# Kernel tuning notes

Hardware: AMD Instinct MI355X
Metric: run time of the kernel (lower is better)

## Reference

```python
import jax, jax.numpy as jnp
import numpy as np

NUM_EMB = 81920
EMB_DIM = 64


def setup_inputs() -> dict:
    key = jax.random.key(0)
    k1, k2 = jax.random.split(key)
    z = jax.random.normal(k1, (4, 8, 8, 8, EMB_DIM), dtype=jnp.float32)
    # faithful to nn.Embedding init: uniform(-1/K, 1/K)
    emb = jax.random.uniform(k2, (NUM_EMB, EMB_DIM), dtype=jnp.float32,
                             minval=-1.0 / NUM_EMB, maxval=1.0 / NUM_EMB)
    return {"z": z, "emb": emb}


def reference(z, emb):
    bs, h, w, d, c = z.shape
    zf = z.reshape(-1, c)  # [N, C]
    # squared euclidean distances; argmin identical to cdist argmin
    # [N, K] = ||z||^2 - 2 z.E^T + ||E||^2
    d2 = (jnp.sum(zf * zf, axis=-1, keepdims=True)
          - 2.0 * jnp.einsum('nc,kc->nk', zf, emb)
          + jnp.sum(emb * emb, axis=-1))
    idx = jnp.argmin(d2, axis=1)  # [N]
    quantized = emb[idx].reshape(bs, h, w, d, c)
    commitment_loss = jnp.mean((z - jax.lax.stop_gradient(quantized)) ** 2)
    vq_loss = jnp.mean((quantized - jax.lax.stop_gradient(z)) ** 2)
    quantized_st = z + jax.lax.stop_gradient(quantized - z)
    return quantized_st, vq_loss, commitment_loss, idx.reshape(bs, h, w, d)
```

## Files before the change

### kernel.cpp

```cpp
#include <hip/hip_runtime.h>
#include <stdint.h>

#define NQ 2048
#define KK 81920
#define CD 64
#define CAP 64
#define DMARG 1.6e-5f
#define QPB 128
#define NSLICE 160
#define SPX 20
#define SPB 5
#define NQBLK 16

#define OUT_VQ 131072
#define OUT_CM 131073
#define OUT_IDX 131074

#define WS_QMAX 0
#define WS_CNT  8192
#define WS_KEYS 16384
#define WS_LOSS 32768
#define WS_CAND 33024
#define WS_ZBF  589824
#define WS_EBF  851968
#define WS_BMAX 11337728

typedef short v8s __attribute__((ext_vector_type(8)));
typedef float v4f __attribute__((ext_vector_type(4)));

__device__ __forceinline__ unsigned int f2o(float f) {
  unsigned int u = __float_as_uint(f);
  return (u & 0x80000000u) ? ~u : (u | 0x80000000u);
}
__device__ __forceinline__ float o2f(unsigned int u) {
  unsigned int v = (u & 0x80000000u) ? (u & 0x7FFFFFFFu) : ~u;
  return __uint_as_float(v);
}
__device__ __forceinline__ unsigned int bf16rne(float f) {
  unsigned int u = __float_as_uint(f);
  u = u + 0x7FFFu + ((u >> 16) & 1u);
  return u >> 16;
}

#define NZ4 32768
#define NTOT4 1343488
__global__ __launch_bounds__(256) void convert_kernel(
    const float* __restrict__ z, const float* __restrict__ emb,
    unsigned int* __restrict__ zbf, unsigned int* __restrict__ ebf,
    int* __restrict__ cnt, float* __restrict__ loss) {
  const int gid = blockIdx.x * 256 + threadIdx.x;
  if (gid < NQ) cnt[gid] = 0;
  if (gid == NQ) *loss = 0.0f;
  const int stride = gridDim.x * 256;
#pragma unroll 1
  for (int i = gid; i < NTOT4; i += stride) {
    const bool isz = (i < NZ4);
    const float4 v = isz ? ((const float4*)z)[i] : ((const float4*)emb)[i - NZ4];
    uint2 o;
    o.x = bf16rne(v.x) | (bf16rne(v.y) << 16);
    o.y = bf16rne(v.z) | (bf16rne(v.w) << 16);
    if (isz) ((uint2*)zbf)[i] = o;
    else     ((uint2*)ebf)[i - NZ4] = o;
  }
}

struct BlkMap { int q0, slice0, xcd, sgrp; };
__device__ __forceinline__ BlkMap decode_block(int bid) {
  BlkMap m;
  m.xcd = bid & 7;
  const int i = bid >> 3;
  const int qblk = i & 15;
  m.sgrp = i >> 4;
  m.q0 = qblk * QPB;
  m.slice0 = m.xcd * SPX + m.sgrp * SPB;
  return m;
}

__device__ __forceinline__ void load_B(v8s (&Bb)[8][2],
                                       const unsigned short* __restrict__ ebf,
                                       int code0, int lrow, int quad) {
#pragma unroll
  for (int cg = 0; cg < 8; ++cg) {
    const unsigned short* er = ebf + (size_t)(code0 + cg * 16 + lrow) * CD + quad * 8;
    Bb[cg][0] = *(const v8s*)er;
    Bb[cg][1] = *(const v8s*)(er + 32);
  }
}

__global__ __launch_bounds__(256, 2) void pass1_kernel(
    const unsigned short* __restrict__ zbf, const unsigned short* __restrict__ ebf,
    unsigned int* __restrict__ bmax) {
  const int tid = threadIdx.x;
  const int wave = tid >> 6, lane = tid & 63;
  const int quad = lane >> 4, lrow = lane & 15;
  const BlkMap bm = decode_block(blockIdx.x);

  v8s A0[8], A1[8];
#pragma unroll
  for (int qg = 0; qg < 8; ++qg) {
    const unsigned short* zr = zbf + (size_t)(bm.q0 + qg * 16 + lrow) * CD + quad * 8;
    A0[qg] = *(const v8s*)zr;
    A1[qg] = *(const v8s*)(zr + 32);
  }

  float pmax[8][4];
#pragma unroll
  for (int qg = 0; qg < 8; ++qg)
#pragma unroll
    for (int r = 0; r < 4; ++r) pmax[qg][r] = -1e30f;

#pragma unroll 1
  for (int s = 0; s < SPB; ++s) {
    v8s B[8][2];
    load_B(B, ebf, (bm.slice0 + s) * 512 + wave * 128, lrow, quad);
#pragma unroll
    for (int qg = 0; qg < 8; ++qg) {
#pragma unroll
      for (int cg = 0; cg < 8; ++cg) {
        v4f acc = {0.f, 0.f, 0.f, 0.f};
        acc = __builtin_amdgcn_mfma_f32_16x16x32_bf16(A0[qg], B[cg][0], acc, 0, 0, 0);
        acc = __builtin_amdgcn_mfma_f32_16x16x32_bf16(A1[qg], B[cg][1], acc, 0, 0, 0);
#pragma unroll
        for (int r = 0; r < 4; ++r) pmax[qg][r] = fmaxf(pmax[qg][r], acc[r]);
      }
    }
  }

#pragma unroll
  for (int m = 1; m <= 8; m <<= 1)
#pragma unroll
    for (int qg = 0; qg < 8; ++qg)
#pragma unroll
      for (int r = 0; r < 4; ++r)
        pmax[qg][r] = fmaxf(pmax[qg][r], __shfl_xor(pmax[qg][r], m, 64));

  __shared__ unsigned int smax[4][QPB];
  if (lrow == 0) {
#pragma unroll
    for (int qg = 0; qg < 8; ++qg) {
      uint4 v;
      v.x = f2o(pmax[qg][0]); v.y = f2o(pmax[qg][1]);
      v.z = f2o(pmax[qg][2]); v.w = f2o(pmax[qg][3]);
      *(uint4*)&smax[wave][qg * 16 + quad * 4] = v;
    }
  }
  __syncthreads();
  if (tid < QPB) {
    unsigned int m0 = smax[0][tid], m1 = smax[1][tid];
    unsigned int m2 = smax[2][tid], m3 = smax[3][tid];
    unsigned int m01 = m0 > m1 ? m0 : m1;
    unsigned int m23 = m2 > m3 ? m2 : m3;
    bmax[(size_t)(bm.q0 + tid) * 32 + bm.xcd * 4 + bm.sgrp] = m01 > m23 ? m01 : m23;
  }
}

__global__ __launch_bounds__(256) void reduce_qmax_kernel(
    const unsigned int* __restrict__ bmax, unsigned int* __restrict__ qmax) {
  const int t = threadIdx.x;
  const int q = blockIdx.x * 8 + (t >> 5);
  const int j = t & 31;
  unsigned int m = bmax[(size_t)q * 32 + j];
#pragma unroll
  for (int s = 16; s; s >>= 1) {
    unsigned int o = (unsigned int)__shfl_xor((int)m, s, 64);
    m = m > o ? m : o;
  }
  if (j == 0) qmax[q] = m;
}

__global__ __launch_bounds__(256, 2) void collect_kernel(
    const unsigned short* __restrict__ zbf, const unsigned short* __restrict__ ebf,
    const unsigned int* __restrict__ qmax, int* __restrict__ cnt,
    int* __restrict__ cand) {
  const int tid = threadIdx.x;
  const int wave = tid >> 6, lane = tid & 63;
  const int quad = lane >> 4, lrow = lane & 15;
  const BlkMap bm = decode_block(blockIdx.x);

  v8s A0[8], A1[8];
#pragma unroll
  for (int qg = 0; qg < 8; ++qg) {
    const unsigned short* zr = zbf + (size_t)(bm.q0 + qg * 16 + lrow) * CD + quad * 8;
    A0[qg] = *(const v8s*)zr;
    A1[qg] = *(const v8s*)(zr + 32);
  }
  float thr[8][4];
#pragma unroll
  for (int qg = 0; qg < 8; ++qg) {
    const uint4 tv = *(const uint4*)(qmax + bm.q0 + qg * 16 + quad * 4);
    thr[qg][0] = o2f(tv.x) - DMARG; thr[qg][1] = o2f(tv.y) - DMARG;
    thr[qg][2] = o2f(tv.z) - DMARG; thr[qg][3] = o2f(tv.w) - DMARG;
  }

#pragma unroll 1
  for (int s = 0; s < SPB; ++s) {
    v8s B[8][2];
    const int scode0 = (bm.slice0 + s) * 512 + wave * 128;
    load_B(B, ebf, scode0, lrow, quad);
#pragma unroll
    for (int qg = 0; qg < 8; ++qg) {
#pragma unroll
      for (int cg = 0; cg < 8; ++cg) {
        v4f acc = {0.f, 0.f, 0.f, 0.f};
        acc = __builtin_amdgcn_mfma_f32_16x16x32_bf16(A0[qg], B[cg][0], acc, 0, 0, 0);
        acc = __builtin_amdgcn_mfma_f32_16x16x32_bf16(A1[qg], B[cg][1], acc, 0, 0, 0);
        const float m01 = fmaxf(acc[0] - thr[qg][0], acc[1] - thr[qg][1]);
        const float m23 = fmaxf(acc[2] - thr[qg][2], acc[3] - thr[qg][3]);
        if (fmaxf(m01, m23) >= 0.0f) {
          const int code = scode0 + cg * 16 + lrow;
#pragma unroll
          for (int r = 0; r < 4; ++r) {
            if (acc[r] >= thr[qg][r]) {
              const int q = bm.q0 + qg * 16 + quad * 4 + r;
              const int pos = atomicAdd(&cnt[q], 1);
              if (pos < CAP) cand[q * CAP + pos] = code;
            }
          }
        }
      }
    }
  }
}

__device__ __forceinline__ unsigned long long exact_key(
    const float* __restrict__ emb, const float zr[CD], float zn2, int k) {
#pragma clang fp contract(off)
  float er[CD];
  const float4* ep = (const float4*)(emb + (size_t)k * CD);
#pragma unroll
  for (int j = 0; j < 16; ++j) {
    float4 v = ep[j];
    er[4 * j] = v.x; er[4 * j + 1] = v.y; er[4 * j + 2] = v.z; er[4 * j + 3] = v.w;
  }
  float acc[16];
#pragma unroll
  for (int j = 0; j < 16; ++j) acc[j] = 0.0f;
#pragma unroll
  for (int q4 = 0; q4 < 16; ++q4) {
    const int jb = 4 * (q4 & 3), cb = 4 * q4;
    acc[jb + 0] = __builtin_fmaf(er[cb + 0], zr[cb + 0], acc[jb + 0]);
    acc[jb + 1] = __builtin_fmaf(er[cb + 1], zr[cb + 1], acc[jb + 1]);
    acc[jb + 2] = __builtin_fmaf(er[cb + 2], zr[cb + 2], acc[jb + 2]);
    acc[jb + 3] = __builtin_fmaf(er[cb + 3], zr[cb + 3], acc[jb + 3]);
  }
  float b8[8], b4[4];
#pragma unroll
  for (int j = 0; j < 8; ++j) b8[j] = acc[j] + acc[j + 8];
#pragma unroll
  for (int j = 0; j < 4; ++j) b4[j] = b8[j] + b8[j + 4];
  const float dot = (b4[0] + b4[2]) + (b4[1] + b4[3]);
  const float t = zn2 - 2.0f * dot;
  return ((unsigned long long)f2o(t) << 32) | (unsigned int)k;
}

__global__ __launch_bounds__(256) void rescore_finalize_kernel(
    const float* __restrict__ z, const float* __restrict__ emb,
    const int* __restrict__ cnt, const int* __restrict__ cand,
    unsigned long long* __restrict__ keys, float* __restrict__ out,
    float* __restrict__ loss) {
#pragma clang fp contract(off)
  const int t = threadIdx.x;
  const int wv = t >> 6, lane = t & 63;
  const int n = blockIdx.x * 4 + wv;

  float zr[CD];
  {
    const float4* zp = (const float4*)(z + (size_t)n * CD);
#pragma unroll
    for (int i = 0; i < 16; ++i) {
      float4 v = zp[i];
      zr[4 * i] = v.x; zr[4 * i + 1] = v.y; zr[4 * i + 2] = v.z; zr[4 * i + 3] = v.w;
    }
  }
  float zn2;
  {
    float r[8];
#pragma unroll
    for (int j = 0; j < 8; ++j) r[j] = zr[j] * zr[j];
#pragma unroll
    for (int i = 8; i < CD; i += 8)
#pragma unroll
      for (int j = 0; j < 8; ++j) r[j] += zr[i + j] * zr[i + j];
    zn2 = ((r[0] + r[1]) + (r[2] + r[3])) + ((r[4] + r[5]) + (r[6] + r[7]));
  }

  const int c = cnt[n];
  unsigned long long best = ~0ull;
  if (c <= CAP) {
    if (lane < c) best = exact_key(emb, zr, zn2, cand[n * CAP + lane]);
  } else {
#pragma unroll 1
    for (int k = lane; k < KK; k += 64) {
      unsigned long long key = exact_key(emb, zr, zn2, k);
      best = (key < best) ? key : best;
    }
  }
#pragma unroll
  for (int m = 32; m; m >>= 1) {
    unsigned long long o = __shfl_xor(best, m, 64);
    best = (o < best) ? o : best;
  }
  const int idx = (int)(best & 0xFFFFFFFFull);
  if (lane == 0) keys[n] = best;

  const float e = emb[(size_t)idx * CD + lane];
  const float zv = z[(size_t)n * CD + lane];
  const float dst = e - zv;
  out[(size_t)n * CD + lane] = zv + dst;
  if (lane == 0) out[OUT_IDX + n] = (float)idx;
  float d = zv - e;
  float sq = d * d;
#pragma unroll
  for (int off = 32; off > 0; off >>= 1) sq += __shfl_down(sq, off, 64);
  __shared__ float part[4];
  if (lane == 0) part[wv] = sq;
  __syncthreads();
  if (t == 0) atomicAdd(loss, part[0] + part[1] + part[2] + part[3]);
}

__global__ void write_losses(const float* __restrict__ loss, float* __restrict__ out) {
  float m = *loss / (float)(NQ * CD);
  out[OUT_VQ] = m;
  out[OUT_CM] = m;
}

extern "C" void kernel_launch(void* const* d_in, const int* in_sizes, int n_in,
                              void* d_out, int out_size, void* d_ws, size_t ws_size,
                              hipStream_t stream) {
  const float* z = (const float*)d_in[0];
  const float* emb = (const float*)d_in[1];
  float* out = (float*)d_out;
  char* ws = (char*)d_ws;
  unsigned int* qmax = (unsigned int*)(ws + WS_QMAX);
  int* cnt = (int*)(ws + WS_CNT);
  unsigned long long* keys = (unsigned long long*)(ws + WS_KEYS);
  float* loss = (float*)(ws + WS_LOSS);
  int* cand = (int*)(ws + WS_CAND);
  unsigned int* zbf = (unsigned int*)(ws + WS_ZBF);
  unsigned int* ebf = (unsigned int*)(ws + WS_EBF);
  unsigned int* bmax = (unsigned int*)(ws + WS_BMAX);

  convert_kernel<<<1312, 256, 0, stream>>>(z, emb, zbf, ebf, cnt, loss);
  pass1_kernel<<<512, 256, 0, stream>>>(
      (const unsigned short*)zbf, (const unsigned short*)ebf, bmax);
  reduce_qmax_kernel<<<NQ / 8, 256, 0, stream>>>(bmax, qmax);
  collect_kernel<<<512, 256, 0, stream>>>(
      (const unsigned short*)zbf, (const unsigned short*)ebf, qmax, cnt, cand);
  rescore_finalize_kernel<<<NQ / 4, 256, 0, stream>>>(z, emb, cnt, cand, keys, out, loss);
  write_losses<<<1, 1, 0, stream>>>(loss, out);
}
```

Before: 152.1 us.

## Double-buffer codebook loads in pass1/collect and fold qmax reduction into collect

Splits each 128-code B tile into two halves and prefetches the next slice's half while MFMAs run on the other, so global loads overlap with compute in both pass1 and collect. It also removes the separate reduce_qmax kernel: each collect block now reduces its 128 queries' 32 partial maxima into shared memory itself. The unused keys write from rescore is dropped. The prefetch keeps two half-tiles live at once, which may raise register pressure under the 2-blocks-per-SM launch bound, and collect redundantly recomputes qmax in every block.

```diff
diff --git a/kernel.cpp b/kernel.cpp
--- a/kernel.cpp
+++ b/kernel.cpp
@@ -76,12 +76,12 @@
   return m;
 }
 
-__device__ __forceinline__ void load_B(v8s (&Bb)[8][2],
-                                       const unsigned short* __restrict__ ebf,
-                                       int code0, int lrow, int quad) {
-#pragma unroll
-  for (int cg = 0; cg < 8; ++cg) {
-    const unsigned short* er = ebf + (size_t)(code0 + cg * 16 + lrow) * CD + quad * 8;
+__device__ __forceinline__ void load_Bhalf(v8s (&Bb)[4][2],
+                                           const unsigned short* __restrict__ ebf,
+                                           int codeh0, int lrow, int quad) {
+#pragma unroll
+  for (int cg = 0; cg < 4; ++cg) {
+    const unsigned short* er = ebf + (size_t)(codeh0 + cg * 16 + lrow) * CD + quad * 8;
     Bb[cg][0] = *(const v8s*)er;
     Bb[cg][1] = *(const v8s*)(er + 32);
   }
@@ -109,21 +109,39 @@
 #pragma unroll
     for (int r = 0; r < 4; ++r) pmax[qg][r] = -1e30f;
 
+  v8s B0[4][2], B1[4][2];
+  {
+    const int c0 = bm.slice0 * 512 + wave * 128;
+    load_Bhalf(B0, ebf, c0, lrow, quad);
+    load_Bhalf(B1, ebf, c0 + 64, lrow, quad);
+  }
 #pragma unroll 1
   for (int s = 0; s < SPB; ++s) {
-    v8s B[8][2];
-    load_B(B, ebf, (bm.slice0 + s) * 512 + wave * 128, lrow, quad);
-#pragma unroll
-    for (int qg = 0; qg < 8; ++qg) {
-#pragma unroll
-      for (int cg = 0; cg < 8; ++cg) {
+    const int cnext = (bm.slice0 + s + 1) * 512 + wave * 128;
+#pragma unroll
+    for (int qg = 0; qg < 8; ++qg) {
+#pragma unroll
+      for (int cg = 0; cg < 4; ++cg) {
         v4f acc = {0.f, 0.f, 0.f, 0.f};
-        acc = __builtin_amdgcn_mfma_f32_16x16x32_bf16(A0[qg], B[cg][0], acc, 0, 0, 0);
-        acc = __builtin_amdgcn_mfma_f32_16x16x32_bf16(A1[qg], B[cg][1], acc, 0, 0, 0);
+        acc = __builtin_amdgcn_mfma_f32_16x16x32_bf16(A0[qg], B0[cg][0], acc, 0, 0, 0);
+        acc = __builtin_amdgcn_mfma_f32_16x16x32_bf16(A1[qg], B0[cg][1], acc, 0, 0, 0);
 #pragma unroll
         for (int r = 0; r < 4; ++r) pmax[qg][r] = fmaxf(pmax[qg][r], acc[r]);
       }
     }
+    if (s + 1 < SPB) load_Bhalf(B0, ebf, cnext, lrow, quad);
+#pragma unroll
+    for (int qg = 0; qg < 8; ++qg) {
+#pragma unroll
+      for (int cg = 0; cg < 4; ++cg) {
+        v4f acc = {0.f, 0.f, 0.f, 0.f};
+        acc = __builtin_amdgcn_mfma_f32_16x16x32_bf16(A0[qg], B1[cg][0], acc, 0, 0, 0);
+        acc = __builtin_amdgcn_mfma_f32_16x16x32_bf16(A1[qg], B1[cg][1], acc, 0, 0, 0);
+#pragma unroll
+        for (int r = 0; r < 4; ++r) pmax[qg][r] = fmaxf(pmax[qg][r], acc[r]);
+      }
+    }
+    if (s + 1 < SPB) load_Bhalf(B1, ebf, cnext + 64, lrow, quad);
   }
 
 #pragma unroll
@@ -154,29 +172,30 @@
   }
 }
 
-__global__ __launch_bounds__(256) void reduce_qmax_kernel(
-    const unsigned int* __restrict__ bmax, unsigned int* __restrict__ qmax) {
-  const int t = threadIdx.x;
-  const int q = blockIdx.x * 8 + (t >> 5);
-  const int j = t & 31;
-  unsigned int m = bmax[(size_t)q * 32 + j];
-#pragma unroll
-  for (int s = 16; s; s >>= 1) {
-    unsigned int o = (unsigned int)__shfl_xor((int)m, s, 64);
-    m = m > o ? m : o;
-  }
-  if (j == 0) qmax[q] = m;
-}
-
 __global__ __launch_bounds__(256, 2) void collect_kernel(
     const unsigned short* __restrict__ zbf, const unsigned short* __restrict__ ebf,
-    const unsigned int* __restrict__ qmax, int* __restrict__ cnt,
+    const unsigned int* __restrict__ bmax, int* __restrict__ cnt,
     int* __restrict__ cand) {
   const int tid = threadIdx.x;
   const int wave = tid >> 6, lane = tid & 63;
   const int quad = lane >> 4, lrow = lane & 15;
   const BlkMap bm = decode_block(blockIdx.x);
 
+  __shared__ unsigned int qmaxl[QPB];
+  if (tid < QPB) {
+    const uint4* bp = (const uint4*)(bmax + (size_t)(bm.q0 + tid) * 32);
+    unsigned int m = 0;
+#pragma unroll
+    for (int j = 0; j < 8; ++j) {
+      uint4 v = bp[j];
+      unsigned int a = v.x > v.y ? v.x : v.y;
+      unsigned int b = v.z > v.w ? v.z : v.w;
+      unsigned int c = a > b ? a : b;
+      m = m > c ? m : c;
+    }
+    qmaxl[tid] = m;
+  }
+
   v8s A0[8], A1[8];
 #pragma unroll
   for (int qg = 0; qg < 8; ++qg) {
@@ -184,26 +203,32 @@
     A0[qg] = *(const v8s*)zr;
     A1[qg] = *(const v8s*)(zr + 32);
   }
+  __syncthreads();
   float thr[8][4];
 #pragma unroll
   for (int qg = 0; qg < 8; ++qg) {
-    const uint4 tv = *(const uint4*)(qmax + bm.q0 + qg * 16 + quad * 4);
+    const uint4 tv = *(const uint4*)&qmaxl[qg * 16 + quad * 4];
     thr[qg][0] = o2f(tv.x) - DMARG; thr[qg][1] = o2f(tv.y) - DMARG;
     thr[qg][2] = o2f(tv.z) - DMARG; thr[qg][3] = o2f(tv.w) - DMARG;
   }
 
+  v8s B0[4][2], B1[4][2];
+  {
+    const int c0 = bm.slice0 * 512 + wave * 128;
+    load_Bhalf(B0, ebf, c0, lrow, quad);
+    load_Bhalf(B1, ebf, c0 + 64, lrow, quad);
+  }
 #pragma unroll 1
   for (int s = 0; s < SPB; ++s) {
-    v8s B[8][2];
     const int scode0 = (bm.slice0 + s) * 512 + wave * 128;
-    load_B(B, ebf, scode0, lrow, quad);
-#pragma unroll
-    for (int qg = 0; qg < 8; ++qg) {
-#pragma unroll
-      for (int cg = 0; cg < 8; ++cg) {
+    const int cnext = scode0 + 512;
+#pragma unroll
+    for (int qg = 0; qg < 8; ++qg) {
+#pragma unroll
+      for (int cg = 0; cg < 4; ++cg) {
         v4f acc = {0.f, 0.f, 0.f, 0.f};
-        acc = __builtin_amdgcn_mfma_f32_16x16x32_bf16(A0[qg], B[cg][0], acc, 0, 0, 0);
-        acc = __builtin_amdgcn_mfma_f32_16x16x32_bf16(A1[qg], B[cg][1], acc, 0, 0, 0);
+        acc = __builtin_amdgcn_mfma_f32_16x16x32_bf16(A0[qg], B0[cg][0], acc, 0, 0, 0);
+        acc = __builtin_amdgcn_mfma_f32_16x16x32_bf16(A1[qg], B0[cg][1], acc, 0, 0, 0);
         const float m01 = fmaxf(acc[0] - thr[qg][0], acc[1] - thr[qg][1]);
         const float m23 = fmaxf(acc[2] - thr[qg][2], acc[3] - thr[qg][3]);
         if (fmaxf(m01, m23) >= 0.0f) {
@@ -219,6 +244,30 @@
         }
       }
     }
+    if (s + 1 < SPB) load_Bhalf(B0, ebf, cnext, lrow, quad);
+#pragma unroll
+    for (int qg = 0; qg < 8; ++qg) {
+#pragma unroll
+      for (int cg = 0; cg < 4; ++cg) {
+        v4f acc = {0.f, 0.f, 0.f, 0.f};
+        acc = __builtin_amdgcn_mfma_f32_16x16x32_bf16(A0[qg], B1[cg][0], acc, 0, 0, 0);
+        acc = __builtin_amdgcn_mfma_f32_16x16x32_bf16(A1[qg], B1[cg][1], acc, 0, 0, 0);
+        const float m01 = fmaxf(acc[0] - thr[qg][0], acc[1] - thr[qg][1]);
+        const float m23 = fmaxf(acc[2] - thr[qg][2], acc[3] - thr[qg][3]);
+        if (fmaxf(m01, m23) >= 0.0f) {
+          const int code = scode0 + 64 + cg * 16 + lrow;
+#pragma unroll
+          for (int r = 0; r < 4; ++r) {
+            if (acc[r] >= thr[qg][r]) {
+              const int q = bm.q0 + qg * 16 + quad * 4 + r;
+              const int pos = atomicAdd(&cnt[q], 1);
+              if (pos < CAP) cand[q * CAP + pos] = code;
+            }
+          }
+        }
+      }
+    }
+    if (s + 1 < SPB) load_Bhalf(B1, ebf, cnext + 64, lrow, quad);
   }
 }
 
@@ -256,8 +305,7 @@
 __global__ __launch_bounds__(256) void rescore_finalize_kernel(
     const float* __restrict__ z, const float* __restrict__ emb,
     const int* __restrict__ cnt, const int* __restrict__ cand,
-    unsigned long long* __restrict__ keys, float* __restrict__ out,
-    float* __restrict__ loss) {
+    float* __restrict__ out, float* __restrict__ loss) {
 #pragma clang fp contract(off)
   const int t = threadIdx.x;
   const int wv = t >> 6, lane = t & 63;
@@ -301,7 +349,6 @@
     best = (o < best) ? o : best;
   }
   const int idx = (int)(best & 0xFFFFFFFFull);
-  if (lane == 0) keys[n] = best;
 
   const float e = emb[(size_t)idx * CD + lane];
   const float zv = z[(size_t)n * CD + lane];
@@ -331,9 +378,7 @@
   const float* emb = (const float*)d_in[1];
   float* out = (float*)d_out;
   char* ws = (char*)d_ws;
-  unsigned int* qmax = (unsigned int*)(ws + WS_QMAX);
   int* cnt = (int*)(ws + WS_CNT);
-  unsigned long long* keys = (unsigned long long*)(ws + WS_KEYS);
   float* loss = (float*)(ws + WS_LOSS);
   int* cand = (int*)(ws + WS_CAND);
   unsigned int* zbf = (unsigned int*)(ws + WS_ZBF);
@@ -343,9 +388,8 @@
   convert_kernel<<<1312, 256, 0, stream>>>(z, emb, zbf, ebf, cnt, loss);
   pass1_kernel<<<512, 256, 0, stream>>>(
       (const unsigned short*)zbf, (const unsigned short*)ebf, bmax);
-  reduce_qmax_kernel<<<NQ / 8, 256, 0, stream>>>(bmax, qmax);
   collect_kernel<<<512, 256, 0, stream>>>(
-      (const unsigned short*)zbf, (const unsigned short*)ebf, qmax, cnt, cand);
-  rescore_finalize_kernel<<<NQ / 4, 256, 0, stream>>>(z, emb, cnt, cand, keys, out, loss);
+      (const unsigned short*)zbf, (const unsigned short*)ebf, bmax, cnt, cand);
+  rescore_finalize_kernel<<<NQ / 4, 256, 0, stream>>>(z, emb, cnt, cand, out, loss);
   write_losses<<<1, 1, 0, stream>>>(loss, out);
 }
```

Measured after the change: 257.9 us. +69.5%, slower.

## Halve queries per block, fuse qmax reduction into collect, drop keys write

Applied to the files above, without the earlier changes.

Queries per block drop from 128 to 64, so the grid doubles to 1024 blocks, and each slice's codes are processed in two halves of 64 to cut register pressure. The separate reduce_qmax kernel is removed. collect_kernel now reduces the 32 per-block maxima for each query into shared memory itself, which saves one launch and a global round trip. The unused keys store in rescore is also dropped. In exchange, each zbf/ebf tile is reused across fewer queries, so more bf16 codebook data is reloaded per MFMA, and each collect block redoes part of the reduction.

```diff
diff --git a/kernel.cpp b/kernel.cpp
--- a/kernel.cpp
+++ b/kernel.cpp
@@ -6,19 +6,17 @@
 #define CD 64
 #define CAP 64
 #define DMARG 1.6e-5f
-#define QPB 128
+#define QPB 64
+#define NQBLK 32
 #define NSLICE 160
 #define SPX 20
 #define SPB 5
-#define NQBLK 16
 
 #define OUT_VQ 131072
 #define OUT_CM 131073
 #define OUT_IDX 131074
 
-#define WS_QMAX 0
 #define WS_CNT  8192
-#define WS_KEYS 16384
 #define WS_LOSS 32768
 #define WS_CAND 33024
 #define WS_ZBF  589824
@@ -69,18 +67,18 @@
   BlkMap m;
   m.xcd = bid & 7;
   const int i = bid >> 3;
-  const int qblk = i & 15;
-  m.sgrp = i >> 4;
+  const int qblk = i & 31;
+  m.sgrp = i >> 5;
   m.q0 = qblk * QPB;
   m.slice0 = m.xcd * SPX + m.sgrp * SPB;
   return m;
 }
 
-__device__ __forceinline__ void load_B(v8s (&Bb)[8][2],
-                                       const unsigned short* __restrict__ ebf,
-                                       int code0, int lrow, int quad) {
-#pragma unroll
-  for (int cg = 0; cg < 8; ++cg) {
+__device__ __forceinline__ void load_B4(v8s (&Bb)[4][2],
+                                        const unsigned short* __restrict__ ebf,
+                                        int code0, int lrow, int quad) {
+#pragma unroll
+  for (int cg = 0; cg < 4; ++cg) {
     const unsigned short* er = ebf + (size_t)(code0 + cg * 16 + lrow) * CD + quad * 8;
     Bb[cg][0] = *(const v8s*)er;
     Bb[cg][1] = *(const v8s*)(er + 32);
@@ -95,33 +93,36 @@
   const int quad = lane >> 4, lrow = lane & 15;
   const BlkMap bm = decode_block(blockIdx.x);
 
-  v8s A0[8], A1[8];
-#pragma unroll
-  for (int qg = 0; qg < 8; ++qg) {
+  v8s A0[4], A1[4];
+#pragma unroll
+  for (int qg = 0; qg < 4; ++qg) {
     const unsigned short* zr = zbf + (size_t)(bm.q0 + qg * 16 + lrow) * CD + quad * 8;
     A0[qg] = *(const v8s*)zr;
     A1[qg] = *(const v8s*)(zr + 32);
   }
 
-  float pmax[8][4];
-#pragma unroll
-  for (int qg = 0; qg < 8; ++qg)
+  float pmax[4][4];
+#pragma unroll
+  for (int qg = 0; qg < 4; ++qg)
 #pragma unroll
     for (int r = 0; r < 4; ++r) pmax[qg][r] = -1e30f;
 
 #pragma unroll 1
   for (int s = 0; s < SPB; ++s) {
-    v8s B[8][2];
-    load_B(B, ebf, (bm.slice0 + s) * 512 + wave * 128, lrow, quad);
-#pragma unroll
-    for (int qg = 0; qg < 8; ++qg) {
-#pragma unroll
-      for (int cg = 0; cg < 8; ++cg) {
-        v4f acc = {0.f, 0.f, 0.f, 0.f};
-        acc = __builtin_amdgcn_mfma_f32_16x16x32_bf16(A0[qg], B[cg][0], acc, 0, 0, 0);
-        acc = __builtin_amdgcn_mfma_f32_16x16x32_bf16(A1[qg], B[cg][1], acc, 0, 0, 0);
-#pragma unroll
-        for (int r = 0; r < 4; ++r) pmax[qg][r] = fmaxf(pmax[qg][r], acc[r]);
+#pragma unroll 1
+    for (int h = 0; h < 2; ++h) {
+      v8s B[4][2];
+      load_B4(B, ebf, (bm.slice0 + s) * 512 + wave * 128 + h * 64, lrow, quad);
+#pragma unroll
+      for (int qg = 0; qg < 4; ++qg) {
+#pragma unroll
+        for (int cg = 0; cg < 4; ++cg) {
+          v4f acc = {0.f, 0.f, 0.f, 0.f};
+          acc = __builtin_amdgcn_mfma_f32_16x16x32_bf16(A0[qg], B[cg][0], acc, 0, 0, 0);
+          acc = __builtin_amdgcn_mfma_f32_16x16x32_bf16(A1[qg], B[cg][1], acc, 0, 0, 0);
+#pragma unroll
+          for (int r = 0; r < 4; ++r) pmax[qg][r] = fmaxf(pmax[qg][r], acc[r]);
+        }
       }
     }
   }
@@ -129,7 +130,7 @@
 #pragma unroll
   for (int m = 1; m <= 8; m <<= 1)
 #pragma unroll
-    for (int qg = 0; qg < 8; ++qg)
+    for (int qg = 0; qg < 4; ++qg)
 #pragma unroll
       for (int r = 0; r < 4; ++r)
         pmax[qg][r] = fmaxf(pmax[qg][r], __shfl_xor(pmax[qg][r], m, 64));
@@ -137,7 +138,7 @@
   __shared__ unsigned int smax[4][QPB];
   if (lrow == 0) {
 #pragma unroll
-    for (int qg = 0; qg < 8; ++qg) {
+    for (int qg = 0; qg < 4; ++qg) {
       uint4 v;
       v.x = f2o(pmax[qg][0]); v.y = f2o(pmax[qg][1]);
       v.z = f2o(pmax[qg][2]); v.w = f2o(pmax[qg][3]);
@@ -154,66 +155,71 @@
   }
 }
 
-__global__ __launch_bounds__(256) void reduce_qmax_kernel(
-    const unsigned int* __restrict__ bmax, unsigned int* __restrict__ qmax) {
-  const int t = threadIdx.x;
-  const int q = blockIdx.x * 8 + (t >> 5);
-  const int j = t & 31;
-  unsigned int m = bmax[(size_t)q * 32 + j];
-#pragma unroll
-  for (int s = 16; s; s >>= 1) {
-    unsigned int o = (unsigned int)__shfl_xor((int)m, s, 64);
-    m = m > o ? m : o;
-  }
-  if (j == 0) qmax[q] = m;
-}
-
 __global__ __launch_bounds__(256, 2) void collect_kernel(
     const unsigned short* __restrict__ zbf, const unsigned short* __restrict__ ebf,
-    const unsigned int* __restrict__ qmax, int* __restrict__ cnt,
+    const unsigned int* __restrict__ bmax, int* __restrict__ cnt,
     int* __restrict__ cand) {
   const int tid = threadIdx.x;
   const int wave = tid >> 6, lane = tid & 63;
   const int quad = lane >> 4, lrow = lane & 15;
   const BlkMap bm = decode_block(blockIdx.x);
 
-  v8s A0[8], A1[8];
-#pragma unroll
-  for (int qg = 0; qg < 8; ++qg) {
+  __shared__ unsigned int qmaxl[QPB];
+  if (tid < QPB) {
+    const uint4* bp = (const uint4*)(bmax + (size_t)(bm.q0 + tid) * 32);
+    unsigned int m = 0;
+#pragma unroll
+    for (int j = 0; j < 8; ++j) {
+      uint4 v = bp[j];
+      unsigned int a = v.x > v.y ? v.x : v.y;
+      unsigned int b = v.z > v.w ? v.z : v.w;
+      unsigned int c = a > b ? a : b;
+      m = m > c ? m : c;
+    }
+    qmaxl[tid] = m;
+  }
+
+  v8s A0[4], A1[4];
+#pragma unroll
+  for (int qg = 0; qg < 4; ++qg) {
     const unsigned short* zr = zbf + (size_t)(bm.q0 + qg * 16 + lrow) * CD + quad * 8;
     A0[qg] = *(const v8s*)zr;
     A1[qg] = *(const v8s*)(zr + 32);
   }
-  float thr[8][4];
-#pragma unroll
-  for (int qg = 0; qg < 8; ++qg) {
-    const uint4 tv = *(const uint4*)(qmax + bm.q0 + qg * 16 + quad * 4);
+  __syncthreads();
+  float thr[4][4];
+#pragma unroll
+  for (int qg = 0; qg < 4; ++qg) {
+    const uint4 tv = *(const uint4*)&qmaxl[qg * 16 + quad * 4];
     thr[qg][0] = o2f(tv.x) - DMARG; thr[qg][1] = o2f(tv.y) - DMARG;
     thr[qg][2] = o2f(tv.z) - DMARG; thr[qg][3] = o2f(tv.w) - DMARG;
   }
 
 #pragma unroll 1
   for (int s = 0; s < SPB; ++s) {
-    v8s B[8][2];
-    const int scode0 = (bm.slice0 + s) * 512 + wave * 128;
-    load_B(B, ebf, scode0, lrow, quad);
-#pragma unroll
-    for (int qg = 0; qg < 8; ++qg) {
-#pragma unroll
-      for (int cg = 0; cg < 8; ++cg) {
-        v4f acc = {0.f, 0.f, 0.f, 0.f};
-        acc = __builtin_amdgcn_mfma_f32_16x16x32_bf16(A0[qg], B[cg][0], acc, 0, 0, 0);
-        acc = __builtin_amdgcn_mfma_f32_16x16x32_bf16(A1[qg], B[cg][1], acc, 0, 0, 0);
-        const float m01 = fmaxf(acc[0] - thr[qg][0], acc[1] - thr[qg][1]);
-        const float m23 = fmaxf(acc[2] - thr[qg][2], acc[3] - thr[qg][3]);
-        if (fmaxf(m01, m23) >= 0.0f) {
-          const int code = scode0 + cg * 16 + lrow;
-#pragma unroll
-          for (int r = 0; r < 4; ++r) {
-            if (acc[r] >= thr[qg][r]) {
-              const int q = bm.q0 + qg * 16 + quad * 4 + r;
-              const int pos = atomicAdd(&cnt[q], 1);
-              if (pos < CAP) cand[q * CAP + pos] = code;
+#pragma unroll 1
+    for (int h = 0; h < 2; ++h) {
+      const int code0 = (bm.slice0 + s) * 512 + wave * 128 + h * 64;
+      v8s B[4][2];
+      load_B4(B, ebf, code0, lrow, quad);
+#pragma unroll
+      for (int qg = 0; qg < 4; ++qg) {
+#pragma unroll
+        for (int cg = 0; cg < 4; ++cg) {
+          v4f acc = {0.f, 0.f, 0.f, 0.f};
+          acc = __builtin_amdgcn_mfma_f32_16x16x32_bf16(A0[qg], B[cg][0], acc, 0, 0, 0);
+          acc = __builtin_amdgcn_mfma_f32_16x16x32_bf16(A1[qg], B[cg][1], acc, 0, 0, 0);
+          const float m01 = fmaxf(acc[0] - thr[qg][0], acc[1] - thr[qg][1]);
+          const float m23 = fmaxf(acc[2] - thr[qg][2], acc[3] - thr[qg][3]);
+          if (fmaxf(m01, m23) >= 0.0f) {
+            const int code = code0 + cg * 16 + lrow;
+#pragma unroll
+            for (int r = 0; r < 4; ++r) {
+              if (acc[r] >= thr[qg][r]) {
+                const int q = bm.q0 + qg * 16 + quad * 4 + r;
+                const int pos = atomicAdd(&cnt[q], 1);
+                if (pos < CAP) cand[q * CAP + pos] = code;
+              }
             }
           }
         }
@@ -256,8 +262,7 @@
 __global__ __launch_bounds__(256) void rescore_finalize_kernel(
     const float* __restrict__ z, const float* __restrict__ emb,
     const int* __restrict__ cnt, const int* __restrict__ cand,
-    unsigned long long* __restrict__ keys, float* __restrict__ out,
-    float* __restrict__ loss) {
+    float* __restrict__ out, float* __restrict__ loss) {
 #pragma clang fp contract(off)
   const int t = threadIdx.x;
   const int wv = t >> 6, lane = t & 63;
@@ -301,7 +306,6 @@
     best = (o < best) ? o : best;
   }
   const int idx = (int)(best & 0xFFFFFFFFull);
-  if (lane == 0) keys[n] = best;
 
   const float e = emb[(size_t)idx * CD + lane];
   const float zv = z[(size_t)n * CD + lane];
@@ -331,9 +335,7 @@
   const float* emb = (const float*)d_in[1];
   float* out = (float*)d_out;
   char* ws = (char*)d_ws;
-  unsigned int* qmax = (unsigned int*)(ws + WS_QMAX);
   int* cnt = (int*)(ws + WS_CNT);
-  unsigned long long* keys = (unsigned long long*)(ws + WS_KEYS);
   float* loss = (float*)(ws + WS_LOSS);
   int* cand = (int*)(ws + WS_CAND);
   unsigned int* zbf = (unsigned int*)(ws + WS_ZBF);
@@ -341,11 +343,11 @@
   unsigned int* bmax = (unsigned int*)(ws + WS_BMAX);
 
   convert_kernel<<<1312, 256, 0, stream>>>(z, emb, zbf, ebf, cnt, loss);
-  pass1_kernel<<<512, 256, 0, stream>>>(
+  const int nblk = NQBLK * (NSLICE / SPB);
+  pass1_kernel<<<nblk, 256, 0, stream>>>(
       (const unsigned short*)zbf, (const unsigned short*)ebf, bmax);
-  reduce_qmax_kernel<<<NQ / 8, 256, 0, stream>>>(bmax, qmax);
-  collect_kernel<<<512, 256, 0, stream>>>(
-      (const unsigned short*)zbf, (const unsigned short*)ebf, qmax, cnt, cand);
-  rescore_finalize_kernel<<<NQ / 4, 256, 0, stream>>>(z, emb, cnt, cand, keys, out, loss);
+  collect_kernel<<<nblk, 256, 0, stream>>>(
+      (const unsigned short*)zbf, (const unsigned short*)ebf, bmax, cnt, cand);
+  rescore_finalize_kernel<<<NQ / 4, 256, 0, stream>>>(z, emb, cnt, cand, out, loss);
   write_losses<<<1, 1, 0, stream>>>(loss, out);
 }
```

Result: slower. 174.1 us (+14.4%).
